# Optimization experiments

Hardware: AMD Instinct MI355X
Metric: run time of the kernel (lower is better)

The kernel has to match this reference:

```python
import jax, jax.numpy as jnp
import numpy as np

NUM_EMBEDDINGS = 1024
EMBEDDING_DIM = 64
COMMITMENT_COST = 0.25


def setup_inputs() -> dict:
    key = jax.random.key(0)
    kz, kc = jax.random.split(key)
    z = jax.random.normal(kz, (16, 2048, EMBEDDING_DIM), dtype=jnp.float32)
    # nn.Embedding weight init: uniform(-1/K, 1/K)
    codebook = (jax.random.uniform(kc, (NUM_EMBEDDINGS, EMBEDDING_DIM), dtype=jnp.float32) * 2.0 - 1.0) / NUM_EMBEDDINGS
    return {"z": z, "codebook": codebook}


def reference(z, codebook):
    D = codebook.shape[1]
    K = codebook.shape[0]
    flat_z = z.reshape(-1, D)  # [N, D]
    # squared L2 distances: ||z||^2 + ||e||^2 - 2 z.e  -> [N, K]
    distances = (
        jnp.sum(flat_z ** 2, axis=1, keepdims=True)
        + jnp.sum(codebook ** 2, axis=1)
        - 2.0 * jnp.matmul(flat_z, codebook.T)
    )
    encoding_indices = jnp.argmin(distances, axis=1)  # [N]
    quantized = codebook[encoding_indices].reshape(z.shape)

    e_latent_loss = jnp.mean((jax.lax.stop_gradient(quantized) - z) ** 2)
    q_latent_loss = jnp.mean((quantized - jax.lax.stop_gradient(z)) ** 2)
    vq_loss = q_latent_loss + COMMITMENT_COST * e_latent_loss

    # straight-through estimator
    quantized_st = z + jax.lax.stop_gradient(quantized - z)

    # perplexity from codebook usage histogram
    n = encoding_indices.shape[0]
    counts = jnp.zeros((K,), dtype=jnp.float32).at[encoding_indices].add(1.0)
    avg_probs = counts / n
    perplexity = jnp.exp(-jnp.sum(avg_probs * jnp.log(avg_probs + 1e-10)))

    indices_out = encoding_indices.reshape(z.shape[:-1])
    return quantized_st, vq_loss, indices_out, perplexity
```

## Files before the change

kernel.cpp:

```cpp
#include <hip/hip_runtime.h>
#include <math.h>


#define D 64
#define KC 1024
#define ROWS 64
#define TC 32
#define NT (KC / TC)
#define NP (NT / 2)
#define BCH 33
#define TILE_SH (16 * BCH * 8)

typedef short short8 __attribute__((ext_vector_type(8)));
typedef short short4v __attribute__((ext_vector_type(4)));
typedef float f32x4 __attribute__((ext_vector_type(4)));

__device__ __forceinline__ unsigned short f2bf(float x) {
  unsigned int u = __float_as_uint(x);
  unsigned int r = (u + 0x7fffu + ((u >> 16) & 1u)) >> 16;
  return (unsigned short)r;
}
__device__ __forceinline__ float bf2f(unsigned short h) {
  return __uint_as_float((unsigned int)h << 16);
}

__device__ __forceinline__ void split8(const float4 a, const float4 b,
                                       short8* hi, short8* lo) {
  float f[8] = {a.x, a.y, a.z, a.w, b.x, b.y, b.z, b.w};
#pragma unroll
  for (int i = 0; i < 8; ++i) {
    unsigned short h = f2bf(f[i]);
    (*hi)[i] = (short)h;
    (*lo)[i] = (short)f2bf(f[i] - bf2f(h));
  }
}

__global__ __launch_bounds__(256) void vq_prep(
    const float* __restrict__ cb, unsigned short* __restrict__ bsplit,
    float* __restrict__ cbn, unsigned int* __restrict__ hist,
    float* __restrict__ loss_acc) {
  const int k = blockIdx.x * 256 + threadIdx.x;
  const float4* e = (const float4*)(cb + (size_t)k * D);
  unsigned short* bp = bsplit + (size_t)k * 128;
  float s0 = 0.f, s1 = 0.f, s2 = 0.f, s3 = 0.f;
#pragma unroll
  for (int i = 0; i < 16; ++i) {
    float4 v = e[i];
    s0 = fmaf(v.x, v.x, s0);
    s1 = fmaf(v.y, v.y, s1);
    s2 = fmaf(v.z, v.z, s2);
    s3 = fmaf(v.w, v.w, s3);
    unsigned short h0 = f2bf(v.x), h1 = f2bf(v.y), h2 = f2bf(v.z), h3 = f2bf(v.w);
    short4v hv = {(short)h0, (short)h1, (short)h2, (short)h3};
    short4v lv = {(short)f2bf(v.x - bf2f(h0)), (short)f2bf(v.y - bf2f(h1)),
                  (short)f2bf(v.z - bf2f(h2)), (short)f2bf(v.w - bf2f(h3))};
    *(short4v*)(bp + i * 4) = hv;
    *(short4v*)(bp + 64 + i * 4) = lv;
  }
  cbn[k] = (s0 + s1) + (s2 + s3);
  hist[k] = 0u;
  if (k == 0) loss_acc[0] = 0.f;
}

__global__ __launch_bounds__(256, 3) void vq_main(
    const float* __restrict__ z, const unsigned short* __restrict__ bsplit,
    const float* __restrict__ cbn, const float* __restrict__ cb,
    float* __restrict__ out_q, float* __restrict__ out_idx,
    unsigned int* __restrict__ hist, float* __restrict__ loss_acc) {
  __shared__ __align__(16) unsigned short Bsh[2][2][TILE_SH];
  __shared__ float scbn[KC];
  __shared__ int skf[ROWS];
  __shared__ float swav[4];
  __shared__ unsigned int lhist[KC];

  const int tid = threadIdx.x;
  const int lane = tid & 63;
  const int wav = tid >> 6;
  const int quad = lane >> 4;
  const int col = lane & 15;
  const int rowbase = blockIdx.x * ROWS;

  const int arow = rowbase + wav * 16 + col;
  const float4* zr = (const float4*)(z + (size_t)arow * D);
  const float4 f0 = zr[quad * 2];
  const float4 f1 = zr[quad * 2 + 1];
  const float4 f2 = zr[8 + quad * 2];
  const float4 f3 = zr[8 + quad * 2 + 1];

  *(float4*)&scbn[tid * 4] = *(const float4*)&cbn[tid * 4];
#pragma unroll
  for (int j = 0; j < KC / 256; ++j) lhist[tid + 256 * j] = 0u;

  const int cslot = (tid & 15) * BCH + (tid >> 4);
#pragma unroll
  for (int T = 0; T < 2; ++T) {
    const size_t off =
        (size_t)(T * TC + (tid >> 4)) * 128 + (size_t)(tid & 15) * 8;
    short8 s0 = *(const short8*)(bsplit + off);
    short8 s1 = *(const short8*)(bsplit + off + 2048);
    *(short8*)&Bsh[0][T][cslot * 8] = s0;
    *(short8*)&Bsh[0][T][(cslot + 16) * 8] = s1;
  }

  short8 a0, a1, a2, a3;
  split8(f0, f1, &a0, &a2);
  split8(f2, f3, &a1, &a3);

  float nrm = ((f0.x * f0.x + f0.y * f0.y) + (f0.z * f0.z + f0.w * f0.w)) +
              ((f1.x * f1.x + f1.y * f1.y) + (f1.z * f1.z + f1.w * f1.w)) +
              ((f2.x * f2.x + f2.y * f2.y) + (f2.z * f2.z + f2.w * f2.w)) +
              ((f3.x * f3.x + f3.y * f3.y) + (f3.z * f3.z + f3.w * f3.w));
  nrm += __shfl_xor(nrm, 16, 64);
  nrm += __shfl_xor(nrm, 32, 64);
  float rzv[4];
#pragma unroll
  for (int r = 0; r < 4; ++r) rzv[r] = __shfl(nrm, quad * 4 + r, 64);

  __syncthreads();

  float b1d[4], b2d[4];
  int b1k[4], b2k[4];
#pragma unroll
  for (int i = 0; i < 4; ++i) {
    b1d[i] = 3.4e38f; b2d[i] = 3.4e38f;
    b1k[i] = 0x7fffffff; b2k[i] = 0x7fffffff;
  }

  for (int p = 0; p < NP; ++p) {
    short8 st00, st01, st10, st11;
    if (p + 1 < NP) {
      const size_t base = (size_t)((p + 1) * 2) * TC;
      const size_t o0 = (base + (tid >> 4)) * 128 + (size_t)(tid & 15) * 8;
      st00 = *(const short8*)(bsplit + o0);
      st01 = *(const short8*)(bsplit + o0 + 2048);
      st10 = *(const short8*)(bsplit + o0 + 4096);
      st11 = *(const short8*)(bsplit + o0 + 6144);
    }
#pragma unroll
    for (int T = 0; T < 2; ++T) {
      const int kb = (p * 2 + T) * TC;
      const unsigned short* bcur = &Bsh[p & 1][T][0];
      const float enA = scbn[kb + col];
      const float enB = scbn[kb + 16 + col];
      const short8 bA0 = *(const short8*)(bcur + ((0 + quad) * BCH + col) * 8);
      const short8 bA1 = *(const short8*)(bcur + ((4 + quad) * BCH + col) * 8);
      const short8 bA2 = *(const short8*)(bcur + ((8 + quad) * BCH + col) * 8);
      const short8 bA3 = *(const short8*)(bcur + ((12 + quad) * BCH + col) * 8);
      const short8 bB0 =
          *(const short8*)(bcur + ((0 + quad) * BCH + col + 16) * 8);
      const short8 bB1 =
          *(const short8*)(bcur + ((4 + quad) * BCH + col + 16) * 8);
      const short8 bB2 =
          *(const short8*)(bcur + ((8 + quad) * BCH + col + 16) * 8);
      const short8 bB3 =
          *(const short8*)(bcur + ((12 + quad) * BCH + col + 16) * 8);

      f32x4 accA = {0.f, 0.f, 0.f, 0.f}, accB = {0.f, 0.f, 0.f, 0.f};
      accA = __builtin_amdgcn_mfma_f32_16x16x32_bf16(a0, bA0, accA, 0, 0, 0);
      accB = __builtin_amdgcn_mfma_f32_16x16x32_bf16(a0, bB0, accB, 0, 0, 0);
      accA = __builtin_amdgcn_mfma_f32_16x16x32_bf16(a1, bA1, accA, 0, 0, 0);
      accB = __builtin_amdgcn_mfma_f32_16x16x32_bf16(a1, bB1, accB, 0, 0, 0);
      accA = __builtin_amdgcn_mfma_f32_16x16x32_bf16(a2, bA0, accA, 0, 0, 0);
      accB = __builtin_amdgcn_mfma_f32_16x16x32_bf16(a2, bB0, accB, 0, 0, 0);
      accA = __builtin_amdgcn_mfma_f32_16x16x32_bf16(a3, bA1, accA, 0, 0, 0);
      accB = __builtin_amdgcn_mfma_f32_16x16x32_bf16(a3, bB1, accB, 0, 0, 0);
      accA = __builtin_amdgcn_mfma_f32_16x16x32_bf16(a0, bA2, accA, 0, 0, 0);
      accB = __builtin_amdgcn_mfma_f32_16x16x32_bf16(a0, bB2, accB, 0, 0, 0);
      accA = __builtin_amdgcn_mfma_f32_16x16x32_bf16(a1, bA3, accA, 0, 0, 0);
      accB = __builtin_amdgcn_mfma_f32_16x16x32_bf16(a1, bB3, accB, 0, 0, 0);

#pragma unroll
      for (int reg = 0; reg < 4; ++reg) {
        {
          float d = fmaf(-2.0f, accA[reg], rzv[reg] + enA);
          int k = kb + col;
          bool w1 = d < b1d[reg];
          bool w2 = d < b2d[reg];
          b2d[reg] = w1 ? b1d[reg] : (w2 ? d : b2d[reg]);
          b2k[reg] = w1 ? b1k[reg] : (w2 ? k : b2k[reg]);
          b1d[reg] = w1 ? d : b1d[reg];
          b1k[reg] = w1 ? k : b1k[reg];
        }
        {
          float d = fmaf(-2.0f, accB[reg], rzv[reg] + enB);
          int k = kb + 16 + col;
          bool w1 = d < b1d[reg];
          bool w2 = d < b2d[reg];
          b2d[reg] = w1 ? b1d[reg] : (w2 ? d : b2d[reg]);
          b2k[reg] = w1 ? b1k[reg] : (w2 ? k : b2k[reg]);
          b1d[reg] = w1 ? d : b1d[reg];
          b1k[reg] = w1 ? k : b1k[reg];
        }
      }
    }

    if (p + 1 < NP) {
      unsigned short* bn0 = &Bsh[(p + 1) & 1][0][0];
      unsigned short* bn1 = &Bsh[(p + 1) & 1][1][0];
      *(short8*)&bn0[cslot * 8] = st00;
      *(short8*)&bn0[(cslot + 16) * 8] = st01;
      *(short8*)&bn1[cslot * 8] = st10;
      *(short8*)&bn1[(cslot + 16) * 8] = st11;
    }
    __syncthreads();
  }

#pragma unroll
  for (int m = 1; m < 16; m <<= 1) {
#pragma unroll
    for (int reg = 0; reg < 4; ++reg) {
      float od1 = __shfl_xor(b1d[reg], m, 64);
      int ok1 = __shfl_xor(b1k[reg], m, 64);
      float od2 = __shfl_xor(b2d[reg], m, 64);
      int ok2 = __shfl_xor(b2k[reg], m, 64);
      bool fo = (od1 < b1d[reg]) || (od1 == b1d[reg] && ok1 < b1k[reg]);
      float w1 = fo ? od1 : b1d[reg];
      int wk1 = fo ? ok1 : b1k[reg];
      float l1 = fo ? b1d[reg] : od1;
      int lk1 = fo ? b1k[reg] : ok1;
      bool so = (od2 < b2d[reg]) || (od2 == b2d[reg] && ok2 < b2k[reg]);
      float m2 = so ? od2 : b2d[reg];
      int mk2 = so ? ok2 : b2k[reg];
      bool lw = (l1 < m2) || (l1 == m2 && lk1 < mk2);
      b1d[reg] = w1;
      b1k[reg] = wk1;
      b2d[reg] = lw ? l1 : m2;
      b2k[reg] = lw ? lk1 : mk2;
    }
  }

  if (col < 4) {
    const int row = wav * 16 + quad * 4 + col;
    float bd1 = b1d[col], bd2 = b2d[col];
    int bk1 = b1k[col], bk2 = b2k[col];
    if (bd2 - bd1 < 1e-5f) {
      const int grow = rowbase + row;
      const float4* zp = (const float4*)(z + (size_t)grow * D);
      float s0 = 0.f, s1 = 0.f, s2 = 0.f, s3 = 0.f;
#pragma unroll
      for (int i = 0; i < 16; ++i) {
        float4 v = zp[i];
        s0 = fmaf(v.x, v.x, s0);
        s1 = fmaf(v.y, v.y, s1);
        s2 = fmaf(v.z, v.z, s2);
        s3 = fmaf(v.w, v.w, s3);
      }
      const float rzx = (s0 + s1) + (s2 + s3);
      float dx[2];
      int kk[2] = {bk1, bk2};
#pragma unroll
      for (int c = 0; c < 2; ++c) {
        const float4* e4 = (const float4*)(cb + (size_t)kk[c] * D);
        float d0 = 0.f, d1 = 0.f, d2 = 0.f, d3 = 0.f;
#pragma unroll
        for (int i = 0; i < 16; ++i) {
          float4 v = e4[i];
          float4 zv = zp[i];
          d0 = fmaf(zv.x, v.x, d0);
          d1 = fmaf(zv.y, v.y, d1);
          d2 = fmaf(zv.z, v.z, d2);
          d3 = fmaf(zv.w, v.w, d3);
        }
        float dot = (d0 + d1) + (d2 + d3);
        dx[c] = (rzx + scbn[kk[c]]) - 2.0f * dot;
      }
      if ((dx[1] < dx[0]) || (dx[1] == dx[0] && bk2 < bk1)) bk1 = bk2;
    }
    skf[row] = bk1;
    out_idx[rowbase + row] = (float)bk1;
    atomicAdd(&lhist[bk1], 1u);
  }
  __syncthreads();

#pragma unroll
  for (int j = 0; j < KC / 256; ++j) {
    unsigned int c = lhist[tid + 256 * j];
    if (c) atomicAdd(&hist[tid + 256 * j], c);
  }

  float lsum = 0.f;
#pragma unroll
  for (int it = 0; it < 4; ++it) {
    int f4 = it * 256 + tid;
    int r = f4 >> 4;
    int c4 = (f4 & 15) * 4;
    int bk = skf[r];
    const float4 q = *(const float4*)(cb + (size_t)bk * D + c4);
    const int grow = rowbase + r;
    const float4 zv = *(const float4*)(z + (size_t)grow * D + c4);
    *(float4*)(out_q + (size_t)grow * D + c4) = q;
    float ax = q.x - zv.x, ay = q.y - zv.y, az = q.z - zv.z, aw = q.w - zv.w;
    lsum += ax * ax + ay * ay + az * az + aw * aw;
  }
#pragma unroll
  for (int off = 32; off > 0; off >>= 1) lsum += __shfl_down(lsum, off, 64);
  if (lane == 0) swav[wav] = lsum;
  __syncthreads();
  if (tid == 0) {
    atomicAdd(loss_acc, (swav[0] + swav[1]) + (swav[2] + swav[3]));
  }
}

__global__ __launch_bounds__(1024) void vq_final(
    const unsigned int* __restrict__ hist, const float* __restrict__ loss_acc,
    float* __restrict__ out_loss, float* __restrict__ out_perp, float inv_n,
    float inv_nd) {
  __shared__ float part[16];
  const int t = threadIdx.x;
  const int lane = t & 63;
  const int wav = t >> 6;
  float p = (float)hist[t] * inv_n;
  float v = p * logf(p + 1e-10f);
#pragma unroll
  for (int off = 32; off > 0; off >>= 1) v += __shfl_down(v, off, 64);
  if (lane == 0) part[wav] = v;
  __syncthreads();
  if (t == 0) {
    float s = 0.f;
#pragma unroll
    for (int j = 0; j < 16; ++j) s += part[j];
    *out_perp = expf(-s);
    *out_loss = 1.25f * loss_acc[0] * inv_nd;
  }
}

extern "C" void kernel_launch(void* const* d_in, const int* in_sizes, int n_in,
                              void* d_out, int out_size, void* d_ws,
                              size_t ws_size, hipStream_t stream) {
  (void)n_in;
  (void)out_size;
  (void)ws_size;
  const float* z = (const float*)d_in[0];
  const float* cb = (const float*)d_in[1];
  const int N = in_sizes[0] / D;

  float* out_q = (float*)d_out;
  float* out_loss = (float*)d_out + (size_t)N * D;
  float* out_idx = out_loss + 1;
  float* out_perp = out_idx + N;

  unsigned int* hist = (unsigned int*)d_ws;
  float* loss_acc = (float*)d_ws + 1024;
  float* cbn = (float*)d_ws + 1040;
  unsigned short* bsplit = (unsigned short*)((float*)d_ws + 2064);

  vq_prep<<<dim3(KC / 256), dim3(256), 0, stream>>>(cb, bsplit, cbn, hist,
                                                    loss_acc);
  vq_main<<<dim3(N / ROWS), dim3(256), 0, stream>>>(z, bsplit, cbn, cb, out_q,
                                                    out_idx, hist, loss_acc);
  vq_final<<<dim3(1), dim3(1024), 0, stream>>>(
      hist, loss_acc, out_loss, out_perp, 1.0f / (float)N,
      1.0f / ((float)N * (float)D));
}
```

Measured before the change: 97.67 us.

## Split codebook tiles across wave pairs, halve rows per block, use global histogram atomics

Each block now handles 32 rows instead of 64, and pairs of waves share a 16-row group with each wave taking one of the two codebook tiles per stage. Their top-2 candidates are merged through shared memory. This doubles the grid and raises the occupancy target, aiming to hide latency better and halve each wave's MFMA/argmin work per stage. The shared histogram is dropped in favour of direct global atomics per row. The cost is loading and staging the codebook twice as often overall, plus more global atomic contention.

```diff
diff --git a/kernel.cpp b/kernel.cpp
--- a/kernel.cpp
+++ b/kernel.cpp
@@ -4,7 +4,7 @@
 
 #define D 64
 #define KC 1024
-#define ROWS 64
+#define ROWS 32
 #define TC 32
 #define NT (KC / TC)
 #define NP (NT / 2)
@@ -62,7 +62,7 @@
   if (k == 0) loss_acc[0] = 0.f;
 }
 
-__global__ __launch_bounds__(256, 3) void vq_main(
+__global__ __launch_bounds__(256, 4) void vq_main(
     const float* __restrict__ z, const unsigned short* __restrict__ bsplit,
     const float* __restrict__ cbn, const float* __restrict__ cb,
     float* __restrict__ out_q, float* __restrict__ out_idx,
@@ -71,16 +71,19 @@
   __shared__ float scbn[KC];
   __shared__ int skf[ROWS];
   __shared__ float swav[4];
-  __shared__ unsigned int lhist[KC];
+  __shared__ float md1[ROWS], md2[ROWS];
+  __shared__ int mkk1[ROWS], mkk2[ROWS];
 
   const int tid = threadIdx.x;
   const int lane = tid & 63;
   const int wav = tid >> 6;
+  const int g = wav >> 1;
+  const int h = wav & 1;
   const int quad = lane >> 4;
   const int col = lane & 15;
   const int rowbase = blockIdx.x * ROWS;
 
-  const int arow = rowbase + wav * 16 + col;
+  const int arow = rowbase + g * 16 + col;
   const float4* zr = (const float4*)(z + (size_t)arow * D);
   const float4 f0 = zr[quad * 2];
   const float4 f1 = zr[quad * 2 + 1];
@@ -88,8 +91,6 @@
   const float4 f3 = zr[8 + quad * 2 + 1];
 
   *(float4*)&scbn[tid * 4] = *(const float4*)&cbn[tid * 4];
-#pragma unroll
-  for (int j = 0; j < KC / 256; ++j) lhist[tid + 256 * j] = 0u;
 
   const int cslot = (tid & 15) * BCH + (tid >> 4);
 #pragma unroll
@@ -136,61 +137,55 @@
       st10 = *(const short8*)(bsplit + o0 + 4096);
       st11 = *(const short8*)(bsplit + o0 + 6144);
     }
-#pragma unroll
-    for (int T = 0; T < 2; ++T) {
-      const int kb = (p * 2 + T) * TC;
-      const unsigned short* bcur = &Bsh[p & 1][T][0];
-      const float enA = scbn[kb + col];
-      const float enB = scbn[kb + 16 + col];
-      const short8 bA0 = *(const short8*)(bcur + ((0 + quad) * BCH + col) * 8);
-      const short8 bA1 = *(const short8*)(bcur + ((4 + quad) * BCH + col) * 8);
-      const short8 bA2 = *(const short8*)(bcur + ((8 + quad) * BCH + col) * 8);
-      const short8 bA3 = *(const short8*)(bcur + ((12 + quad) * BCH + col) * 8);
-      const short8 bB0 =
-          *(const short8*)(bcur + ((0 + quad) * BCH + col + 16) * 8);
-      const short8 bB1 =
-          *(const short8*)(bcur + ((4 + quad) * BCH + col + 16) * 8);
-      const short8 bB2 =
-          *(const short8*)(bcur + ((8 + quad) * BCH + col + 16) * 8);
-      const short8 bB3 =
-          *(const short8*)(bcur + ((12 + quad) * BCH + col + 16) * 8);
-
-      f32x4 accA = {0.f, 0.f, 0.f, 0.f}, accB = {0.f, 0.f, 0.f, 0.f};
-      accA = __builtin_amdgcn_mfma_f32_16x16x32_bf16(a0, bA0, accA, 0, 0, 0);
-      accB = __builtin_amdgcn_mfma_f32_16x16x32_bf16(a0, bB0, accB, 0, 0, 0);
-      accA = __builtin_amdgcn_mfma_f32_16x16x32_bf16(a1, bA1, accA, 0, 0, 0);
-      accB = __builtin_amdgcn_mfma_f32_16x16x32_bf16(a1, bB1, accB, 0, 0, 0);
-      accA = __builtin_amdgcn_mfma_f32_16x16x32_bf16(a2, bA0, accA, 0, 0, 0);
-      accB = __builtin_amdgcn_mfma_f32_16x16x32_bf16(a2, bB0, accB, 0, 0, 0);
-      accA = __builtin_amdgcn_mfma_f32_16x16x32_bf16(a3, bA1, accA, 0, 0, 0);
-      accB = __builtin_amdgcn_mfma_f32_16x16x32_bf16(a3, bB1, accB, 0, 0, 0);
-      accA = __builtin_amdgcn_mfma_f32_16x16x32_bf16(a0, bA2, accA, 0, 0, 0);
-      accB = __builtin_amdgcn_mfma_f32_16x16x32_bf16(a0, bB2, accB, 0, 0, 0);
-      accA = __builtin_amdgcn_mfma_f32_16x16x32_bf16(a1, bA3, accA, 0, 0, 0);
-      accB = __builtin_amdgcn_mfma_f32_16x16x32_bf16(a1, bB3, accB, 0, 0, 0);
-
-#pragma unroll
-      for (int reg = 0; reg < 4; ++reg) {
-        {
-          float d = fmaf(-2.0f, accA[reg], rzv[reg] + enA);
-          int k = kb + col;
-          bool w1 = d < b1d[reg];
-          bool w2 = d < b2d[reg];
-          b2d[reg] = w1 ? b1d[reg] : (w2 ? d : b2d[reg]);
-          b2k[reg] = w1 ? b1k[reg] : (w2 ? k : b2k[reg]);
-          b1d[reg] = w1 ? d : b1d[reg];
-          b1k[reg] = w1 ? k : b1k[reg];
-        }
-        {
-          float d = fmaf(-2.0f, accB[reg], rzv[reg] + enB);
-          int k = kb + 16 + col;
-          bool w1 = d < b1d[reg];
-          bool w2 = d < b2d[reg];
-          b2d[reg] = w1 ? b1d[reg] : (w2 ? d : b2d[reg]);
-          b2k[reg] = w1 ? b1k[reg] : (w2 ? k : b2k[reg]);
-          b1d[reg] = w1 ? d : b1d[reg];
-          b1k[reg] = w1 ? k : b1k[reg];
-        }
+
+    const int kb = (p * 2 + h) * TC;
+    const unsigned short* bcur = &Bsh[p & 1][h][0];
+    const float enA = scbn[kb + col];
+    const float enB = scbn[kb + 16 + col];
+    const short8 bA0 = *(const short8*)(bcur + ((0 + quad) * BCH + col) * 8);
+    const short8 bA1 = *(const short8*)(bcur + ((4 + quad) * BCH + col) * 8);
+    const short8 bA2 = *(const short8*)(bcur + ((8 + quad) * BCH + col) * 8);
+    const short8 bA3 = *(const short8*)(bcur + ((12 + quad) * BCH + col) * 8);
+    const short8 bB0 = *(const short8*)(bcur + ((0 + quad) * BCH + col + 16) * 8);
+    const short8 bB1 = *(const short8*)(bcur + ((4 + quad) * BCH + col + 16) * 8);
+    const short8 bB2 = *(const short8*)(bcur + ((8 + quad) * BCH + col + 16) * 8);
+    const short8 bB3 = *(const short8*)(bcur + ((12 + quad) * BCH + col + 16) * 8);
+
+    f32x4 accA = {0.f, 0.f, 0.f, 0.f}, accB = {0.f, 0.f, 0.f, 0.f};
+    accA = __builtin_amdgcn_mfma_f32_16x16x32_bf16(a0, bA0, accA, 0, 0, 0);
+    accB = __builtin_amdgcn_mfma_f32_16x16x32_bf16(a0, bB0, accB, 0, 0, 0);
+    accA = __builtin_amdgcn_mfma_f32_16x16x32_bf16(a1, bA1, accA, 0, 0, 0);
+    accB = __builtin_amdgcn_mfma_f32_16x16x32_bf16(a1, bB1, accB, 0, 0, 0);
+    accA = __builtin_amdgcn_mfma_f32_16x16x32_bf16(a2, bA0, accA, 0, 0, 0);
+    accB = __builtin_amdgcn_mfma_f32_16x16x32_bf16(a2, bB0, accB, 0, 0, 0);
+    accA = __builtin_amdgcn_mfma_f32_16x16x32_bf16(a3, bA1, accA, 0, 0, 0);
+    accB = __builtin_amdgcn_mfma_f32_16x16x32_bf16(a3, bB1, accB, 0, 0, 0);
+    accA = __builtin_amdgcn_mfma_f32_16x16x32_bf16(a0, bA2, accA, 0, 0, 0);
+    accB = __builtin_amdgcn_mfma_f32_16x16x32_bf16(a0, bB2, accB, 0, 0, 0);
+    accA = __builtin_amdgcn_mfma_f32_16x16x32_bf16(a1, bA3, accA, 0, 0, 0);
+    accB = __builtin_amdgcn_mfma_f32_16x16x32_bf16(a1, bB3, accB, 0, 0, 0);
+
+#pragma unroll
+    for (int reg = 0; reg < 4; ++reg) {
+      {
+        float d = fmaf(-2.0f, accA[reg], rzv[reg] + enA);
+        int k = kb + col;
+        bool w1 = d < b1d[reg];
+        bool w2 = d < b2d[reg];
+        b2d[reg] = w1 ? b1d[reg] : (w2 ? d : b2d[reg]);
+        b2k[reg] = w1 ? b1k[reg] : (w2 ? k : b2k[reg]);
+        b1d[reg] = w1 ? d : b1d[reg];
+        b1k[reg] = w1 ? k : b1k[reg];
+      }
+      {
+        float d = fmaf(-2.0f, accB[reg], rzv[reg] + enB);
+        int k = kb + 16 + col;
+        bool w1 = d < b1d[reg];
+        bool w2 = d < b2d[reg];
+        b2d[reg] = w1 ? b1d[reg] : (w2 ? d : b2d[reg]);
+        b2k[reg] = w1 ? b1k[reg] : (w2 ? k : b2k[reg]);
+        b1d[reg] = w1 ? d : b1d[reg];
+        b1k[reg] = w1 ? k : b1k[reg];
       }
     }
 
@@ -229,10 +224,38 @@
     }
   }
 
-  if (col < 4) {
-    const int row = wav * 16 + quad * 4 + col;
+  if (h == 1 && col < 4) {
+    const int row = g * 16 + quad * 4 + col;
+    md1[row] = b1d[col];
+    mkk1[row] = b1k[col];
+    md2[row] = b2d[col];
+    mkk2[row] = b2k[col];
+  }
+  __syncthreads();
+
+  if (h == 0 && col < 4) {
+    const int row = g * 16 + quad * 4 + col;
     float bd1 = b1d[col], bd2 = b2d[col];
     int bk1 = b1k[col], bk2 = b2k[col];
+    {
+      float od1 = md1[row];
+      int ok1 = mkk1[row];
+      float od2 = md2[row];
+      int ok2 = mkk2[row];
+      bool fo = (od1 < bd1) || (od1 == bd1 && ok1 < bk1);
+      float w1 = fo ? od1 : bd1;
+      int wk1 = fo ? ok1 : bk1;
+      float l1 = fo ? bd1 : od1;
+      int lk1 = fo ? bk1 : ok1;
+      bool so = (od2 < bd2) || (od2 == bd2 && ok2 < bk2);
+      float m2 = so ? od2 : bd2;
+      int mk2v = so ? ok2 : bk2;
+      bool lw = (l1 < m2) || (l1 == m2 && lk1 < mk2v);
+      bd1 = w1;
+      bk1 = wk1;
+      bd2 = lw ? l1 : m2;
+      bk2 = lw ? lk1 : mk2v;
+    }
     if (bd2 - bd1 < 1e-5f) {
       const int grow = rowbase + row;
       const float4* zp = (const float4*)(z + (size_t)grow * D);
@@ -268,19 +291,13 @@
     }
     skf[row] = bk1;
     out_idx[rowbase + row] = (float)bk1;
-    atomicAdd(&lhist[bk1], 1u);
-  }
-  __syncthreads();
-
-#pragma unroll
-  for (int j = 0; j < KC / 256; ++j) {
-    unsigned int c = lhist[tid + 256 * j];
-    if (c) atomicAdd(&hist[tid + 256 * j], c);
-  }
+    atomicAdd(&hist[bk1], 1u);
+  }
+  __syncthreads();
 
   float lsum = 0.f;
 #pragma unroll
-  for (int it = 0; it < 4; ++it) {
+  for (int it = 0; it < 2; ++it) {
     int f4 = it * 256 + tid;
     int r = f4 >> 4;
     int c4 = (f4 & 15) * 4;
```

After: 144.5 us. 47.9% more time.

## Deepen codebook tile prefetch to two pairs ahead with register double-buffering

Applied to the files above, without the earlier changes.

The main loop is unrolled by two, with two register sets (sA/sB) holding global loads of codebook tiles issued two tile-pairs ahead rather than one. Shared-memory buffer slots are now fixed per half-iteration. Launch bounds drop from 3 to 2 blocks per SM, which gives the compiler more registers for the extra prefetch state. This aims to hide more global-load latency, at the cost of lower occupancy and higher register pressure.

```diff
diff --git a/kernel.cpp b/kernel.cpp
--- a/kernel.cpp
+++ b/kernel.cpp
@@ -62,7 +62,7 @@
   if (k == 0) loss_acc[0] = 0.f;
 }
 
-__global__ __launch_bounds__(256, 3) void vq_main(
+__global__ __launch_bounds__(256, 2) void vq_main(
     const float* __restrict__ z, const unsigned short* __restrict__ bsplit,
     const float* __restrict__ cbn, const float* __restrict__ cb,
     float* __restrict__ out_q, float* __restrict__ out_idx,
@@ -92,6 +92,7 @@
   for (int j = 0; j < KC / 256; ++j) lhist[tid + 256 * j] = 0u;
 
   const int cslot = (tid & 15) * BCH + (tid >> 4);
+
 #pragma unroll
   for (int T = 0; T < 2; ++T) {
     const size_t off =
@@ -102,6 +103,17 @@
     *(short8*)&Bsh[0][T][(cslot + 16) * 8] = s1;
   }
 
+  short8 sB0, sB1, sB2, sB3;
+  {
+    const size_t o0 = ((size_t)(1 * 2 * TC) + (tid >> 4)) * 128 +
+                      (size_t)(tid & 15) * 8;
+    sB0 = *(const short8*)(bsplit + o0);
+    sB1 = *(const short8*)(bsplit + o0 + 2048);
+    sB2 = *(const short8*)(bsplit + o0 + 4096);
+    sB3 = *(const short8*)(bsplit + o0 + 6144);
+  }
+  short8 sA0, sA1, sA2, sA3;
+
   short8 a0, a1, a2, a3;
   split8(f0, f1, &a0, &a2);
   split8(f2, f3, &a1, &a3);
@@ -126,20 +138,11 @@
     b1k[i] = 0x7fffffff; b2k[i] = 0x7fffffff;
   }
 
-  for (int p = 0; p < NP; ++p) {
-    short8 st00, st01, st10, st11;
-    if (p + 1 < NP) {
-      const size_t base = (size_t)((p + 1) * 2) * TC;
-      const size_t o0 = (base + (tid >> 4)) * 128 + (size_t)(tid & 15) * 8;
-      st00 = *(const short8*)(bsplit + o0);
-      st01 = *(const short8*)(bsplit + o0 + 2048);
-      st10 = *(const short8*)(bsplit + o0 + 4096);
-      st11 = *(const short8*)(bsplit + o0 + 6144);
-    }
+  auto compute_pair = [&](int p, int slot) {
 #pragma unroll
     for (int T = 0; T < 2; ++T) {
       const int kb = (p * 2 + T) * TC;
-      const unsigned short* bcur = &Bsh[p & 1][T][0];
+      const unsigned short* bcur = &Bsh[slot][T][0];
       const float enA = scbn[kb + col];
       const float enB = scbn[kb + 16 + col];
       const short8 bA0 = *(const short8*)(bcur + ((0 + quad) * BCH + col) * 8);
@@ -193,14 +196,47 @@
         }
       }
     }
-
-    if (p + 1 < NP) {
-      unsigned short* bn0 = &Bsh[(p + 1) & 1][0][0];
-      unsigned short* bn1 = &Bsh[(p + 1) & 1][1][0];
-      *(short8*)&bn0[cslot * 8] = st00;
-      *(short8*)&bn0[(cslot + 16) * 8] = st01;
-      *(short8*)&bn1[cslot * 8] = st10;
-      *(short8*)&bn1[(cslot + 16) * 8] = st11;
+  };
+
+  for (int pp = 0; pp < NP / 2; ++pp) {
+    const int p0 = 2 * pp;
+    const int p1 = 2 * pp + 1;
+
+    if (p0 + 2 < NP) {
+      const size_t o0 = ((size_t)(p0 + 2) * 2 * TC + (tid >> 4)) * 128 +
+                        (size_t)(tid & 15) * 8;
+      sA0 = *(const short8*)(bsplit + o0);
+      sA1 = *(const short8*)(bsplit + o0 + 2048);
+      sA2 = *(const short8*)(bsplit + o0 + 4096);
+      sA3 = *(const short8*)(bsplit + o0 + 6144);
+    }
+    compute_pair(p0, 0);
+    {
+      unsigned short* bn0 = &Bsh[1][0][0];
+      unsigned short* bn1 = &Bsh[1][1][0];
+      *(short8*)&bn0[cslot * 8] = sB0;
+      *(short8*)&bn0[(cslot + 16) * 8] = sB1;
+      *(short8*)&bn1[cslot * 8] = sB2;
+      *(short8*)&bn1[(cslot + 16) * 8] = sB3;
+    }
+    __syncthreads();
+
+    if (p1 + 2 < NP) {
+      const size_t o0 = ((size_t)(p1 + 2) * 2 * TC + (tid >> 4)) * 128 +
+                        (size_t)(tid & 15) * 8;
+      sB0 = *(const short8*)(bsplit + o0);
+      sB1 = *(const short8*)(bsplit + o0 + 2048);
+      sB2 = *(const short8*)(bsplit + o0 + 4096);
+      sB3 = *(const short8*)(bsplit + o0 + 6144);
+    }
+    compute_pair(p1, 1);
+    if (p1 + 1 < NP) {
+      unsigned short* bn0 = &Bsh[0][0][0];
+      unsigned short* bn1 = &Bsh[0][1][0];
+      *(short8*)&bn0[cslot * 8] = sA0;
+      *(short8*)&bn0[(cslot + 16) * 8] = sA1;
+      *(short8*)&bn1[cslot * 8] = sA2;
+      *(short8*)&bn1[(cslot + 16) * 8] = sA3;
     }
     __syncthreads();
   }
```

After: 99.12 us. About the same (+1.5%).

## Fuse final reduction into main kernel and drop row-norm from distance

Applied to the files above, without the earlier changes.

Removes the separate vq_final launch by having the last block to finish (tracked by an atomic counter) compute perplexity and loss. Drops the per-row ||z||^2 term from the distance, since it is constant per row and does not change the argmin, along with its shuffles. Uses fminf/fmaxf for the top-2 distance tracking and lowers the launch-bounds occupancy hint from 3 to 2. Risks include the memory ordering of the last-block pattern and changed tie-breaking or rounding near the top-2 boundary, which a later refinement may depend on.

```diff
diff --git a/kernel.cpp b/kernel.cpp
--- a/kernel.cpp
+++ b/kernel.cpp
@@ -38,7 +38,7 @@
 __global__ __launch_bounds__(256) void vq_prep(
     const float* __restrict__ cb, unsigned short* __restrict__ bsplit,
     float* __restrict__ cbn, unsigned int* __restrict__ hist,
-    float* __restrict__ loss_acc) {
+    float* __restrict__ loss_acc, unsigned int* __restrict__ done) {
   const int k = blockIdx.x * 256 + threadIdx.x;
   const float4* e = (const float4*)(cb + (size_t)k * D);
   unsigned short* bp = bsplit + (size_t)k * 128;
@@ -59,19 +59,26 @@
   }
   cbn[k] = (s0 + s1) + (s2 + s3);
   hist[k] = 0u;
-  if (k == 0) loss_acc[0] = 0.f;
-}
-
-__global__ __launch_bounds__(256, 3) void vq_main(
+  if (k == 0) {
+    loss_acc[0] = 0.f;
+    done[0] = 0u;
+  }
+}
+
+__global__ __launch_bounds__(256, 2) void vq_main(
     const float* __restrict__ z, const unsigned short* __restrict__ bsplit,
     const float* __restrict__ cbn, const float* __restrict__ cb,
     float* __restrict__ out_q, float* __restrict__ out_idx,
-    unsigned int* __restrict__ hist, float* __restrict__ loss_acc) {
+    unsigned int* __restrict__ hist, float* __restrict__ loss_acc,
+    unsigned int* __restrict__ done, float* __restrict__ out_loss,
+    float* __restrict__ out_perp, float inv_n, float inv_nd) {
   __shared__ __align__(16) unsigned short Bsh[2][2][TILE_SH];
   __shared__ float scbn[KC];
   __shared__ int skf[ROWS];
   __shared__ float swav[4];
   __shared__ unsigned int lhist[KC];
+  __shared__ float part[16];
+  __shared__ int lastFlag;
 
   const int tid = threadIdx.x;
   const int lane = tid & 63;
@@ -105,16 +112,6 @@
   short8 a0, a1, a2, a3;
   split8(f0, f1, &a0, &a2);
   split8(f2, f3, &a1, &a3);
-
-  float nrm = ((f0.x * f0.x + f0.y * f0.y) + (f0.z * f0.z + f0.w * f0.w)) +
-              ((f1.x * f1.x + f1.y * f1.y) + (f1.z * f1.z + f1.w * f1.w)) +
-              ((f2.x * f2.x + f2.y * f2.y) + (f2.z * f2.z + f2.w * f2.w)) +
-              ((f3.x * f3.x + f3.y * f3.y) + (f3.z * f3.z + f3.w * f3.w));
-  nrm += __shfl_xor(nrm, 16, 64);
-  nrm += __shfl_xor(nrm, 32, 64);
-  float rzv[4];
-#pragma unroll
-  for (int r = 0; r < 4; ++r) rzv[r] = __shfl(nrm, quad * 4 + r, 64);
 
   __syncthreads();
 
@@ -172,23 +169,25 @@
 #pragma unroll
       for (int reg = 0; reg < 4; ++reg) {
         {
-          float d = fmaf(-2.0f, accA[reg], rzv[reg] + enA);
+          float d = fmaf(-2.0f, accA[reg], enA);
           int k = kb + col;
           bool w1 = d < b1d[reg];
           bool w2 = d < b2d[reg];
-          b2d[reg] = w1 ? b1d[reg] : (w2 ? d : b2d[reg]);
+          float nb2 = fminf(fmaxf(d, b1d[reg]), b2d[reg]);
           b2k[reg] = w1 ? b1k[reg] : (w2 ? k : b2k[reg]);
-          b1d[reg] = w1 ? d : b1d[reg];
+          b2d[reg] = nb2;
+          b1d[reg] = fminf(d, b1d[reg]);
           b1k[reg] = w1 ? k : b1k[reg];
         }
         {
-          float d = fmaf(-2.0f, accB[reg], rzv[reg] + enB);
+          float d = fmaf(-2.0f, accB[reg], enB);
           int k = kb + 16 + col;
           bool w1 = d < b1d[reg];
           bool w2 = d < b2d[reg];
-          b2d[reg] = w1 ? b1d[reg] : (w2 ? d : b2d[reg]);
+          float nb2 = fminf(fmaxf(d, b1d[reg]), b2d[reg]);
           b2k[reg] = w1 ? b1k[reg] : (w2 ? k : b2k[reg]);
-          b1d[reg] = w1 ? d : b1d[reg];
+          b2d[reg] = nb2;
+          b1d[reg] = fminf(d, b1d[reg]);
           b1k[reg] = w1 ? k : b1k[reg];
         }
       }
@@ -298,29 +297,31 @@
   __syncthreads();
   if (tid == 0) {
     atomicAdd(loss_acc, (swav[0] + swav[1]) + (swav[2] + swav[3]));
-  }
-}
-
-__global__ __launch_bounds__(1024) void vq_final(
-    const unsigned int* __restrict__ hist, const float* __restrict__ loss_acc,
-    float* __restrict__ out_loss, float* __restrict__ out_perp, float inv_n,
-    float inv_nd) {
-  __shared__ float part[16];
-  const int t = threadIdx.x;
-  const int lane = t & 63;
-  const int wav = t >> 6;
-  float p = (float)hist[t] * inv_n;
-  float v = p * logf(p + 1e-10f);
-#pragma unroll
-  for (int off = 32; off > 0; off >>= 1) v += __shfl_down(v, off, 64);
-  if (lane == 0) part[wav] = v;
+    asm volatile("s_waitcnt vmcnt(0)" ::: "memory");
+    unsigned int t = atomicAdd(done, 1u);
+    lastFlag = (t == (unsigned int)(gridDim.x - 1)) ? 1 : 0;
+  }
   __syncthreads();
-  if (t == 0) {
-    float s = 0.f;
-#pragma unroll
-    for (int j = 0; j < 16; ++j) s += part[j];
-    *out_perp = expf(-s);
-    *out_loss = 1.25f * loss_acc[0] * inv_nd;
+
+  if (lastFlag) {
+#pragma unroll
+    for (int j = 0; j < KC / 256; ++j) {
+      unsigned int c = atomicAdd(&hist[tid + 256 * j], 0u);
+      float pr = (float)c * inv_n;
+      float v = pr * logf(pr + 1e-10f);
+#pragma unroll
+      for (int off = 32; off > 0; off >>= 1) v += __shfl_down(v, off, 64);
+      if (lane == 0) part[wav + 4 * j] = v;
+    }
+    __syncthreads();
+    if (tid == 0) {
+      float s = 0.f;
+#pragma unroll
+      for (int j = 0; j < 16; ++j) s += part[j];
+      float la = atomicAdd(loss_acc, 0.0f);
+      *out_perp = expf(-s);
+      *out_loss = 1.25f * la * inv_nd;
+    }
   }
 }
 
@@ -341,14 +342,13 @@
 
   unsigned int* hist = (unsigned int*)d_ws;
   float* loss_acc = (float*)d_ws + 1024;
+  unsigned int* done = (unsigned int*)d_ws + 1025;
   float* cbn = (float*)d_ws + 1040;
   unsigned short* bsplit = (unsigned short*)((float*)d_ws + 2064);
 
   vq_prep<<<dim3(KC / 256), dim3(256), 0, stream>>>(cb, bsplit, cbn, hist,
-                                                    loss_acc);
-  vq_main<<<dim3(N / ROWS), dim3(256), 0, stream>>>(z, bsplit, cbn, cb, out_q,
-                                                    out_idx, hist, loss_acc);
-  vq_final<<<dim3(1), dim3(1024), 0, stream>>>(
-      hist, loss_acc, out_loss, out_perp, 1.0f / (float)N,
-      1.0f / ((float)N * (float)D));
-}
+                                                    loss_acc, done);
+  vq_main<<<dim3(N / ROWS), dim3(256), 0, stream>>>(
+      z, bsplit, cbn, cb, out_q, out_idx, hist, loss_acc, done, out_loss,
+      out_perp, 1.0f / (float)N, 1.0f / ((float)N * (float)D));
+}
```

Measured after the change: 108.7 us. 1.11x slower.
